# Kernel optimization log

Measured on AMD Instinct MI355X. Metric: run time of the kernel, lower is better.

## Reference

```python
import jax, jax.numpy as jnp
import numpy as np


def setup_inputs() -> dict:
    key = jax.random.key(0)
    x = jax.random.normal(key, (128, 256, 32, 32), dtype=jnp.float32)
    return {"x": x, "iter_num": 5}


def reference(x, iter_num):
    # x: (B, C, H, W)
    B, C, H, W = x.shape
    N = H * W
    xr = x.reshape(B, C, N)
    # Covariance pooling: X @ I_hat @ X^T == (1/N) * Xc @ Xc^T  (I_hat = I/N - J/N^2)
    xc = xr - xr.mean(axis=2, keepdims=True)
    cov = jnp.einsum('bcn,bdn->bcd', xc, xc) / N  # (B, C, C)

    # Newton-Schulz iterative matrix square root
    I = jnp.eye(C, dtype=x.dtype)
    I3 = 3.0 * I
    trace = jnp.trace(cov, axis1=1, axis2=2)[:, None, None]  # norm_A = tr(cov)
    A = cov / trace
    ZY = 0.5 * (I3 - A)
    Y = A @ ZY
    Z = ZY
    for _ in range(1, iter_num - 1):
        ZY = 0.5 * (I3 - Z @ Y)
        Y = Y @ ZY
        Z = ZY @ Z
    YZY = 0.5 * (Y @ (I3 - Z @ Y))
    sqrtm = YZY * jnp.sqrt(trace)  # (B, C, C)

    # Upper-triangular vectorization (row-major, including diagonal)
    r, c = np.triu_indices(C)
    idx = jnp.asarray(r * C + c)
    return sqrtm.reshape(B, C * C)[:, idx]  # (B, C*(C+1)//2)
```

## Files before the change

kernel.cpp:

```cpp
#include <hip/hip_runtime.h>
#include <hip/hip_fp16.h>


typedef _Float16 half8 __attribute__((ext_vector_type(8)));
typedef _Float16 half4 __attribute__((ext_vector_type(4)));
typedef float f32x4 __attribute__((ext_vector_type(4)));

#define OUTPB 32896

__device__ __forceinline__ void gl_lds16(const void* g, void* l) {
  __builtin_amdgcn_global_load_lds(
      (const __attribute__((address_space(1))) void*)g,
      (__attribute__((address_space(3))) void*)l, 16, 0, 0);
}

#define VMB(N) asm volatile("s_waitcnt vmcnt(" #N ")\n\ts_barrier" ::: "memory")
#define LKB()  asm volatile("s_waitcnt lgkmcnt(0)\n\ts_barrier" ::: "memory")

__device__ __forceinline__ void tile_pq(int t, int& p, int& q) {
  p = (t > 3) + (t > 6) + (t > 8);
  int base = p * 4 - (p * (p - 1)) / 2;
  q = p + (t - base);
}

__device__ __forceinline__ half8 cvt8(float4 a, float4 b) {
  half8 h;
  h[0] = (_Float16)a.x; h[1] = (_Float16)a.y; h[2] = (_Float16)a.z; h[3] = (_Float16)a.w;
  h[4] = (_Float16)b.x; h[5] = (_Float16)b.y; h[6] = (_Float16)b.z; h[7] = (_Float16)b.w;
  return h;
}

__device__ __forceinline__ void mfma64(const _Float16* lA, const _Float16* lB,
                                       f32x4 (&acc)[2][2], int wr, int wc,
                                       int lr, int lk) {
#pragma unroll
  for (int ks = 0; ks < 2; ++ks) {
    half8 af[2], bf[2];
#pragma unroll
    for (int m = 0; m < 2; ++m) {
      int row = wr * 32 + m * 16 + lr;
      int kc = (ks * 4 + lk) ^ (row & 7);
      af[m] = *(const half8*)&lA[row * 64 + kc * 8];
    }
#pragma unroll
    for (int n = 0; n < 2; ++n) {
      int row = wc * 32 + n * 16 + lr;
      int kc = (ks * 4 + lk) ^ (row & 7);
      bf[n] = *(const half8*)&lB[row * 64 + kc * 8];
    }
    __builtin_amdgcn_s_setprio(1);
#pragma unroll
    for (int m = 0; m < 2; ++m)
#pragma unroll
      for (int n = 0; n < 2; ++n)
        acc[m][n] = __builtin_amdgcn_mfma_f32_16x16x32_f16(af[m], bf[n], acc[m][n], 0, 0, 0);
    __builtin_amdgcn_s_setprio(0);
  }
}

template <typename F>
__device__ __forceinline__ void store_sym(F f, _Float16* D, size_t boff, int p, int q,
    bool mirror, _Float16* ldsT, f32x4 (&acc)[2][2],
    int wr, int wc, int lr, int lk, int tid) {
#pragma unroll
  for (int m = 0; m < 2; ++m)
#pragma unroll
    for (int n = 0; n < 2; ++n) {
      int il0 = wr * 32 + m * 16 + lk * 4;
      int jl = wc * 32 + n * 16 + lr;
      half4 v4;
#pragma unroll
      for (int r = 0; r < 4; ++r) {
        _Float16 v = f(acc[m][n][r], p * 64 + il0 + r, q * 64 + jl);
        v4[r] = v;
        if (mirror) ldsT[(il0 + r) * 64 + (jl ^ (((il0 + r) & 7) << 3))] = v;
      }
      *(half4*)&D[boff + (size_t)(q * 64 + jl) * 256 + p * 64 + il0] = v4;
    }
  if (mirror) {
    __syncthreads();
#pragma unroll
    for (int pp = 0; pp < 2; ++pp) {
      int u = pp * 256 + tid;
      int im = u >> 3, cu = u & 7;
      half8 v8 = *(const half8*)&ldsT[im * 64 + ((cu ^ (im & 7)) << 3)];
      *(half8*)&D[boff + (size_t)(p * 64 + im) * 256 + q * 64 + cu * 8] = v8;
    }
  }
}

__global__ __launch_bounds__(256, 2) void k_cov(const float* __restrict__ x,
                                                _Float16* __restrict__ covh,
                                                float* __restrict__ trPart) {
  __shared__ _Float16 lds[32768];
  __shared__ float sred[4];

  const int lin = blockIdx.x + 3 * blockIdx.y;
  const int cid = (lin & 7) * 48 + (lin >> 3);
  const int b = cid / 3, t = cid - 3 * b;
  const int p = (t == 1), q = (t != 0);
  const bool diag = (t < 2);
  const int tid = threadIdx.x, w = tid >> 6, lane = tid & 63;
  const int wr = w >> 1, wc = w & 1, lr = lane & 15, lk = lane >> 4;

  const float* Ab = x + ((size_t)b * 256 + p * 128) * 1024;
  const float* Bb = x + ((size_t)b * 256 + q * 128) * 1024;

  float4 la[4][2], lb[4][2];
  f32x4 acc[4][4] = {};
  f32x4 rsA[4] = {}, rsB[4] = {};
  half8 ones;
#pragma unroll
  for (int i = 0; i < 8; ++i) ones[i] = (_Float16)1.0f;

  auto LOAD = [&](int kk) {
#pragma unroll
    for (int i = 0; i < 4; ++i) {
      int u = i * 256 + tid;
      int row = u >> 3, c8 = u & 7;
      int kc = c8 ^ (row & 7);
      const float* sa = Ab + (size_t)row * 1024 + kk * 64 + kc * 8;
      la[i][0] = *(const float4*)sa; la[i][1] = *(const float4*)(sa + 4);
      if (!diag) {
        const float* sb = Bb + (size_t)row * 1024 + kk * 64 + kc * 8;
        lb[i][0] = *(const float4*)sb; lb[i][1] = *(const float4*)(sb + 4);
      }
    }
  };
  auto WRITE = [&](int buf) {
#pragma unroll
    for (int i = 0; i < 4; ++i) {
      int u = i * 256 + tid;
      *(half8*)&lds[buf * 8192 + u * 8] = cvt8(la[i][0], la[i][1]);
      if (!diag) *(half8*)&lds[16384 + buf * 8192 + u * 8] = cvt8(lb[i][0], lb[i][1]);
    }
  };
  auto STEP = [&](const _Float16* lA, const _Float16* lB) {
#pragma unroll
    for (int ks = 0; ks < 2; ++ks) {
      half8 af[4], bf[4];
#pragma unroll
      for (int m = 0; m < 4; ++m) {
        int row = wr * 64 + m * 16 + lr;
        int kc = (ks * 4 + lk) ^ (row & 7);
        af[m] = *(const half8*)&lA[row * 64 + kc * 8];
      }
#pragma unroll
      for (int n = 0; n < 4; ++n) {
        int row = wc * 64 + n * 16 + lr;
        int kc = (ks * 4 + lk) ^ (row & 7);
        bf[n] = *(const half8*)&lB[row * 64 + kc * 8];
      }
      __builtin_amdgcn_s_setprio(1);
#pragma unroll
      for (int m = 0; m < 4; ++m)
        rsA[m] = __builtin_amdgcn_mfma_f32_16x16x32_f16(af[m], ones, rsA[m], 0, 0, 0);
#pragma unroll
      for (int n = 0; n < 4; ++n)
        rsB[n] = __builtin_amdgcn_mfma_f32_16x16x32_f16(ones, bf[n], rsB[n], 0, 0, 0);
#pragma unroll
      for (int m = 0; m < 4; ++m)
#pragma unroll
        for (int n = 0; n < 4; ++n)
          acc[m][n] = __builtin_amdgcn_mfma_f32_16x16x32_f16(af[m], bf[n], acc[m][n], 0, 0, 0);
      __builtin_amdgcn_s_setprio(0);
    }
  };

  LOAD(0); WRITE(0); LOAD(1);
  __syncthreads();
#pragma unroll 1
  for (int kk = 0; kk < 16; ++kk) {
    int cur = kk & 1;
    STEP(&lds[cur * 8192], diag ? &lds[cur * 8192] : &lds[16384 + cur * 8192]);
    if (kk < 15) {
      WRITE(cur ^ 1);
      if (kk < 14) LOAD(kk + 2);
    }
    __syncthreads();
  }

  const float inv = 1.f / 1024.f;
  if (diag) {
    float tp = 0.f;
#pragma unroll
    for (int m = 0; m < 4; ++m)
#pragma unroll
      for (int n = 0; n < 4; ++n)
#pragma unroll
        for (int r = 0; r < 4; ++r) {
          int il = wr * 64 + m * 16 + lk * 4 + r, jl = wc * 64 + n * 16 + lr;
          if (il == jl) tp += (acc[m][n][r] - rsA[m][r] * rsB[n][0] * inv) * inv;
        }
#pragma unroll
    for (int o = 32; o; o >>= 1) tp += __shfl_down(tp, o);
    if (lane == 0) sred[w] = tp;
    __syncthreads();
    if (tid == 0) trPart[b * 2 + p] = sred[0] + sred[1] + sred[2] + sred[3];
  }

  const size_t boff = (size_t)b * 65536;
#pragma unroll
  for (int m = 0; m < 4; ++m)
#pragma unroll
    for (int n = 0; n < 4; ++n) {
      int il0 = wr * 64 + m * 16 + lk * 4;
      int jl = wc * 64 + n * 16 + lr;
      half4 v4;
#pragma unroll
      for (int r = 0; r < 4; ++r) {
        int il = il0 + r;
        float cv = (acc[m][n][r] - rsA[m][r] * rsB[n][0] * inv) * inv;
        v4[r] = (_Float16)cv;
        if (!diag) lds[il * 128 + (((jl >> 3) ^ (il & 7)) << 3) + (jl & 7)] = v4[r];
      }
      *(half4*)&covh[boff + (size_t)(q * 128 + jl) * 256 + p * 128 + il0] = v4;
    }
  if (!diag) {
    __syncthreads();
#pragma unroll
    for (int pp = 0; pp < 8; ++pp) {
      int u = pp * 256 + tid;
      int im = u >> 4, cu = u & 15;
      half8 v8 = *(const half8*)&lds[im * 128 + ((cu ^ (im & 7)) << 3)];
      *(half8*)&covh[boff + (size_t)(p * 128 + im) * 256 + q * 128 + cu * 8] = v8;
    }
  }
}

enum { EPI_S2 = 0, EPI_ZY = 1, EPI_OUT = 2 };

struct GP {
  const _Float16 *A0, *B0;
  _Float16 *D0, *D1;
  const _Float16* covh;
  const float* trP;
  float* outF;
};

template <int EPI>
__global__ __launch_bounds__(256, 4) void k_gemm(GP g) {
  __shared__ _Float16 lds[16384];

  const int lin = blockIdx.x + 10 * blockIdx.y;
  const int cid = (lin & 7) * 160 + (lin >> 3);
  const int b = cid / 10, t = cid - 10 * b;
  int p, q; tile_pq(t, p, q);
  const bool diag = (p == q);
  const bool share = diag && (EPI == EPI_S2);
  const int tid = threadIdx.x, w = tid >> 6, lane = tid & 63;
  const int wr = w >> 1, wc = w & 1, lr = lane & 15, lk = lane >> 4;

  const size_t boff = (size_t)b * 65536;
  const _Float16* Ap = g.A0 + boff + (size_t)p * 64 * 256;
  const _Float16* Bp = ((EPI == EPI_S2) ? g.A0 : g.B0) + boff + (size_t)q * 64 * 256;

  f32x4 acc[2][2] = {};

  auto stageH = [&](const _Float16* panel, int buf, int base, int kk) {
#pragma unroll
    for (int i = 0; i < 2; ++i) {
      int s = (w * 2 + i) * 64 + lane;
      int row = s >> 3, cst = s & 7;
      int kc = cst ^ (row & 7);
      gl_lds16(panel + (size_t)row * 256 + kk * 64 + kc * 8,
               &lds[base + buf * 4096 + (w * 2 + i) * 512]);
    }
  };

  stageH(Ap, 0, 0, 0);
  if (!share) stageH(Bp, 0, 8192, 0);
#pragma unroll 1
  for (int kk = 0; kk < 4; ++kk) {
    int cur = kk & 1;
    if (kk < 3) {
      stageH(Ap, cur ^ 1, 0, kk + 1);
      if (!share) {
        stageH(Bp, cur ^ 1, 8192, kk + 1);
        VMB(4);
      } else {
        VMB(2);
      }
    } else {
      VMB(0);
    }
    mfma64(&lds[cur * 4096], share ? &lds[cur * 4096] : &lds[8192 + cur * 4096],
           acc, wr, wc, lr, lk);
    LKB();
  }

  if constexpr (EPI == EPI_ZY) {
    store_sym([&](float a, int i, int j) {
                return (_Float16)((i == j ? 1.5f : 0.f) - 0.5f * a);
              }, g.D0, boff, p, q, !diag, lds, acc, wr, wc, lr, lk, tid);
  } else if constexpr (EPI == EPI_S2) {
    float tv = g.trP[b * 2] + g.trP[b * 2 + 1];
    float it1 = 1.f / tv;
    _Float16* TY = lds;
    _Float16* TZ = lds + 4096;
#pragma unroll
    for (int m = 0; m < 2; ++m)
#pragma unroll
      for (int n = 0; n < 2; ++n) {
        int il0 = wr * 32 + m * 16 + lk * 4;
        int jl = wc * 32 + n * 16 + lr;
        half4 c4 = *(const half4*)&g.covh[boff + (size_t)(q * 64 + jl) * 256 + p * 64 + il0];
        half4 y4, z4;
#pragma unroll
        for (int r = 0; r < 4; ++r) {
          int i = p * 64 + il0 + r, j = q * 64 + jl;
          float c = (float)c4[r];
          y4[r] = (_Float16)(1.5f * c * it1 - 0.5f * acc[m][n][r] * it1 * it1);
          z4[r] = (_Float16)((i == j ? 1.5f : 0.f) - 0.5f * c * it1);
          if (!diag) {
            int sp = (il0 + r) * 64 + (jl ^ (((il0 + r) & 7) << 3));
            TY[sp] = y4[r]; TZ[sp] = z4[r];
          }
        }
        *(half4*)&g.D0[boff + (size_t)(q * 64 + jl) * 256 + p * 64 + il0] = y4;
        *(half4*)&g.D1[boff + (size_t)(q * 64 + jl) * 256 + p * 64 + il0] = z4;
      }
    if (!diag) {
      __syncthreads();
#pragma unroll
      for (int pp = 0; pp < 2; ++pp) {
        int u = pp * 256 + tid;
        int im = u >> 3, cu = u & 7;
        half8 vy = *(const half8*)&TY[im * 64 + ((cu ^ (im & 7)) << 3)];
        half8 vz = *(const half8*)&TZ[im * 64 + ((cu ^ (im & 7)) << 3)];
        *(half8*)&g.D0[boff + (size_t)(p * 64 + im) * 256 + q * 64 + cu * 8] = vy;
        *(half8*)&g.D1[boff + (size_t)(p * 64 + im) * 256 + q * 64 + cu * 8] = vz;
      }
    }
  } else {
    float tv = g.trP[b * 2] + g.trP[b * 2 + 1];
    float st = sqrtf(tv);
#pragma unroll
    for (int m = 0; m < 2; ++m)
#pragma unroll
      for (int n = 0; n < 2; ++n)
#pragma unroll
        for (int r = 0; r < 4; ++r) {
          int i = p * 64 + wr * 32 + m * 16 + lk * 4 + r;
          int j = q * 64 + wc * 32 + n * 16 + lr;
          if (i <= j) {
            int idx = j + i * 256 - (i * (i + 1)) / 2;
            g.outF[(size_t)b * OUTPB + idx] = acc[m][n][r] * st;
          }
        }
  }
}

struct YZP {
  const _Float16 *Y, *Z, *W;
  _Float16 *Yn, *Zn;
};

__global__ __launch_bounds__(256, 3) void k_yzm(YZP g) {
  __shared__ _Float16 lds[24576];

  const int lin = blockIdx.x + 10 * blockIdx.y;
  const int cid = (lin & 7) * 160 + (lin >> 3);
  const int b = cid / 10, t = cid - 10 * b;
  int p, q; tile_pq(t, p, q);
  const bool diag = (p == q);
  const int tid = threadIdx.x, w = tid >> 6, lane = tid & 63;
  const int wr = w >> 1, wc = w & 1, lr = lane & 15, lk = lane >> 4;

  const size_t boff = (size_t)b * 65536;
  const _Float16* Yp = g.Y + boff + (size_t)p * 64 * 256;
  const _Float16* Zp = g.Z + boff + (size_t)p * 64 * 256;
  const _Float16* Wp = g.W + boff + (size_t)q * 64 * 256;

  f32x4 accY[2][2] = {}, accZ[2][2] = {};

  auto stageH = [&](const _Float16* panel, int buf, int base, int kk) {
#pragma unroll
    for (int i = 0; i < 2; ++i) {
      int s = (w * 2 + i) * 64 + lane;
      int row = s >> 3, cst = s & 7;
      int kc = cst ^ (row & 7);
      gl_lds16(panel + (size_t)row * 256 + kk * 64 + kc * 8,
               &lds[base + buf * 4096 + (w * 2 + i) * 512]);
    }
  };

  auto step = [&](const _Float16* lY, const _Float16* lZ, const _Float16* lW) {
#pragma unroll
    for (int ks = 0; ks < 2; ++ks) {
      half8 yf[2], zf[2], wf[2];
#pragma unroll
      for (int m = 0; m < 2; ++m) {
        int row = wr * 32 + m * 16 + lr;
        int kc = (ks * 4 + lk) ^ (row & 7);
        yf[m] = *(const half8*)&lY[row * 64 + kc * 8];
        zf[m] = *(const half8*)&lZ[row * 64 + kc * 8];
      }
#pragma unroll
      for (int n = 0; n < 2; ++n) {
        int row = wc * 32 + n * 16 + lr;
        int kc = (ks * 4 + lk) ^ (row & 7);
        wf[n] = *(const half8*)&lW[row * 64 + kc * 8];
      }
      __builtin_amdgcn_s_setprio(1);
#pragma unroll
      for (int m = 0; m < 2; ++m)
#pragma unroll
        for (int n = 0; n < 2; ++n) {
          accY[m][n] = __builtin_amdgcn_mfma_f32_16x16x32_f16(yf[m], wf[n], accY[m][n], 0, 0, 0);
          accZ[m][n] = __builtin_amdgcn_mfma_f32_16x16x32_f16(zf[m], wf[n], accZ[m][n], 0, 0, 0);
        }
      __builtin_amdgcn_s_setprio(0);
    }
  };

  stageH(Yp, 0, 0, 0); stageH(Zp, 0, 8192, 0); stageH(Wp, 0, 16384, 0);
#pragma unroll 1
  for (int kk = 0; kk < 4; ++kk) {
    int cur = kk & 1;
    if (kk < 3) {
      stageH(Yp, cur ^ 1, 0, kk + 1);
      stageH(Zp, cur ^ 1, 8192, kk + 1);
      stageH(Wp, cur ^ 1, 16384, kk + 1);
      VMB(6);
    } else {
      VMB(0);
    }
    step(&lds[cur * 4096], &lds[8192 + cur * 4096], &lds[16384 + cur * 4096]);
    LKB();
  }

  _Float16* TY = lds;
  _Float16* TZ = lds + 4096;
#pragma unroll
  for (int m = 0; m < 2; ++m)
#pragma unroll
    for (int n = 0; n < 2; ++n) {
      int il0 = wr * 32 + m * 16 + lk * 4;
      int jl = wc * 32 + n * 16 + lr;
      half4 y4, z4;
#pragma unroll
      for (int r = 0; r < 4; ++r) {
        y4[r] = (_Float16)accY[m][n][r];
        z4[r] = (_Float16)accZ[m][n][r];
        if (!diag) {
          int sp = (il0 + r) * 64 + (jl ^ (((il0 + r) & 7) << 3));
          TY[sp] = y4[r]; TZ[sp] = z4[r];
        }
      }
      *(half4*)&g.Yn[boff + (size_t)(q * 64 + jl) * 256 + p * 64 + il0] = y4;
      *(half4*)&g.Zn[boff + (size_t)(q * 64 + jl) * 256 + p * 64 + il0] = z4;
    }
  if (!diag) {
    __syncthreads();
#pragma unroll
    for (int pp = 0; pp < 2; ++pp) {
      int u = pp * 256 + tid;
      int im = u >> 3, cu = u & 7;
      half8 vy = *(const half8*)&TY[im * 64 + ((cu ^ (im & 7)) << 3)];
      half8 vz = *(const half8*)&TZ[im * 64 + ((cu ^ (im & 7)) << 3)];
      *(half8*)&g.Yn[boff + (size_t)(p * 64 + im) * 256 + q * 64 + cu * 8] = vy;
      *(half8*)&g.Zn[boff + (size_t)(p * 64 + im) * 256 + q * 64 + cu * 8] = vz;
    }
  }
}

extern "C" void kernel_launch(void* const* d_in, const int* in_sizes, int n_in,
                              void* d_out, int out_size, void* d_ws, size_t ws_size,
                              hipStream_t stream) {
  const float* x = (const float*)d_in[0];
  float* outF = (float*)d_out;

  char* ws = (char*)d_ws;
  const size_t MATB = (size_t)128 * 65536 * sizeof(_Float16);
  _Float16* covh = (_Float16*)ws;
  _Float16* Y0   = (_Float16*)(ws + MATB);
  _Float16* Z0   = (_Float16*)(ws + 2 * MATB);
  _Float16* Y1   = (_Float16*)(ws + 3 * MATB);
  _Float16* Z1   = (_Float16*)(ws + 4 * MATB);
  float* trP     = (float*)(ws + 5 * MATB);

  dim3 g3(3, 128), g10(10, 128);

  k_cov<<<g3, 256, 0, stream>>>(x, covh, trP);

  {
    GP a{};
    a.A0 = covh; a.D0 = Y0; a.D1 = Z0;
    a.covh = covh; a.trP = trP;
    k_gemm<EPI_S2><<<g10, 256, 0, stream>>>(a);
  }

  _Float16 *Yc = Y0, *Zc = Z0, *Yn = Y1, *Zn = Z1;
  for (int itn = 0; itn < 3; ++itn) {
    GP a{};
    a.A0 = Zc; a.B0 = Yc; a.D0 = covh;
    k_gemm<EPI_ZY><<<g10, 256, 0, stream>>>(a);
    YZP r{};
    r.Y = Yc; r.Z = Zc; r.W = covh; r.Yn = Yn; r.Zn = Zn;
    k_yzm<<<g10, 256, 0, stream>>>(r);
    _Float16* t0 = Yc; Yc = Yn; Yn = t0;
    _Float16* t1 = Zc; Zc = Zn; Zn = t1;
  }
  {
    GP a{};
    a.A0 = Zc; a.B0 = Yc; a.D0 = covh;
    k_gemm<EPI_ZY><<<g10, 256, 0, stream>>>(a);
    GP o{};
    o.A0 = Yc; o.B0 = covh; o.trP = trP; o.outF = outF;
    k_gemm<EPI_OUT><<<g10, 256, 0, stream>>>(o);
  }
}
```

Measured before the change: 159.0 us.

## Fuse each Newton-Schulz iteration into one column-panel kernel

Replaces the two-kernel-per-iteration scheme (ZY = 1.5I - 0.5 Z@Y written to global, then Y@ZY and ZY@Z) with a single kernel per iteration. Each block owns a 64-column panel of one batch: it computes the ZY panel into LDS, then multiplies Y and Z by it, and writes the new Y and Z columns. This removes the global round trip of ZY and half the launches. The cost is that symmetric-tile reuse is lost, so full 256x64 panels are computed with a 4x128 grid at lower occupancy, and the Y and Z panels are streamed again for each column block.

```diff
diff --git a/kernel.cpp b/kernel.cpp
--- a/kernel.cpp
+++ b/kernel.cpp
@@ -58,205 +58,9 @@
   }
 }
 
-template <typename F>
-__device__ __forceinline__ void store_sym(F f, _Float16* D, size_t boff, int p, int q,
-    bool mirror, _Float16* ldsT, f32x4 (&acc)[2][2],
-    int wr, int wc, int lr, int lk, int tid) {
-#pragma unroll
-  for (int m = 0; m < 2; ++m)
-#pragma unroll
-    for (int n = 0; n < 2; ++n) {
-      int il0 = wr * 32 + m * 16 + lk * 4;
-      int jl = wc * 32 + n * 16 + lr;
-      half4 v4;
-#pragma unroll
-      for (int r = 0; r < 4; ++r) {
-        _Float16 v = f(acc[m][n][r], p * 64 + il0 + r, q * 64 + jl);
-        v4[r] = v;
-        if (mirror) ldsT[(il0 + r) * 64 + (jl ^ (((il0 + r) & 7) << 3))] = v;
-      }
-      *(half4*)&D[boff + (size_t)(q * 64 + jl) * 256 + p * 64 + il0] = v4;
-    }
-  if (mirror) {
-    __syncthreads();
-#pragma unroll
-    for (int pp = 0; pp < 2; ++pp) {
-      int u = pp * 256 + tid;
-      int im = u >> 3, cu = u & 7;
-      half8 v8 = *(const half8*)&ldsT[im * 64 + ((cu ^ (im & 7)) << 3)];
-      *(half8*)&D[boff + (size_t)(p * 64 + im) * 256 + q * 64 + cu * 8] = v8;
-    }
-  }
-}
-
-__global__ __launch_bounds__(256, 2) void k_cov(const float* __restrict__ x,
-                                                _Float16* __restrict__ covh,
-                                                float* __restrict__ trPart) {
-  __shared__ _Float16 lds[32768];
-  __shared__ float sred[4];
-
-  const int lin = blockIdx.x + 3 * blockIdx.y;
-  const int cid = (lin & 7) * 48 + (lin >> 3);
-  const int b = cid / 3, t = cid - 3 * b;
-  const int p = (t == 1), q = (t != 0);
-  const bool diag = (t < 2);
-  const int tid = threadIdx.x, w = tid >> 6, lane = tid & 63;
-  const int wr = w >> 1, wc = w & 1, lr = lane & 15, lk = lane >> 4;
-
-  const float* Ab = x + ((size_t)b * 256 + p * 128) * 1024;
-  const float* Bb = x + ((size_t)b * 256 + q * 128) * 1024;
-
-  float4 la[4][2], lb[4][2];
-  f32x4 acc[4][4] = {};
-  f32x4 rsA[4] = {}, rsB[4] = {};
-  half8 ones;
-#pragma unroll
-  for (int i = 0; i < 8; ++i) ones[i] = (_Float16)1.0f;
-
-  auto LOAD = [&](int kk) {
-#pragma unroll
-    for (int i = 0; i < 4; ++i) {
-      int u = i * 256 + tid;
-      int row = u >> 3, c8 = u & 7;
-      int kc = c8 ^ (row & 7);
-      const float* sa = Ab + (size_t)row * 1024 + kk * 64 + kc * 8;
-      la[i][0] = *(const float4*)sa; la[i][1] = *(const float4*)(sa + 4);
-      if (!diag) {
-        const float* sb = Bb + (size_t)row * 1024 + kk * 64 + kc * 8;
-        lb[i][0] = *(const float4*)sb; lb[i][1] = *(const float4*)(sb + 4);
-      }
-    }
-  };
-  auto WRITE = [&](int buf) {
-#pragma unroll
-    for (int i = 0; i < 4; ++i) {
-      int u = i * 256 + tid;
-      *(half8*)&lds[buf * 8192 + u * 8] = cvt8(la[i][0], la[i][1]);
-      if (!diag) *(half8*)&lds[16384 + buf * 8192 + u * 8] = cvt8(lb[i][0], lb[i][1]);
-    }
-  };
-  auto STEP = [&](const _Float16* lA, const _Float16* lB) {
-#pragma unroll
-    for (int ks = 0; ks < 2; ++ks) {
-      half8 af[4], bf[4];
-#pragma unroll
-      for (int m = 0; m < 4; ++m) {
-        int row = wr * 64 + m * 16 + lr;
-        int kc = (ks * 4 + lk) ^ (row & 7);
-        af[m] = *(const half8*)&lA[row * 64 + kc * 8];
-      }
-#pragma unroll
-      for (int n = 0; n < 4; ++n) {
-        int row = wc * 64 + n * 16 + lr;
-        int kc = (ks * 4 + lk) ^ (row & 7);
-        bf[n] = *(const half8*)&lB[row * 64 + kc * 8];
-      }
-      __builtin_amdgcn_s_setprio(1);
-#pragma unroll
-      for (int m = 0; m < 4; ++m)
-        rsA[m] = __builtin_amdgcn_mfma_f32_16x16x32_f16(af[m], ones, rsA[m], 0, 0, 0);
-#pragma unroll
-      for (int n = 0; n < 4; ++n)
-        rsB[n] = __builtin_amdgcn_mfma_f32_16x16x32_f16(ones, bf[n], rsB[n], 0, 0, 0);
-#pragma unroll
-      for (int m = 0; m < 4; ++m)
-#pragma unroll
-        for (int n = 0; n < 4; ++n)
-          acc[m][n] = __builtin_amdgcn_mfma_f32_16x16x32_f16(af[m], bf[n], acc[m][n], 0, 0, 0);
-      __builtin_amdgcn_s_setprio(0);
-    }
-  };
-
-  LOAD(0); WRITE(0); LOAD(1);
-  __syncthreads();
-#pragma unroll 1
-  for (int kk = 0; kk < 16; ++kk) {
-    int cur = kk & 1;
-    STEP(&lds[cur * 8192], diag ? &lds[cur * 8192] : &lds[16384 + cur * 8192]);
-    if (kk < 15) {
-      WRITE(cur ^ 1);
-      if (kk < 14) LOAD(kk + 2);
-    }
-    __syncthreads();
-  }
-
-  const float inv = 1.f / 1024.f;
-  if (diag) {
-    float tp = 0.f;
-#pragma unroll
-    for (int m = 0; m < 4; ++m)
-#pragma unroll
-      for (int n = 0; n < 4; ++n)
-#pragma unroll
-        for (int r = 0; r < 4; ++r) {
-          int il = wr * 64 + m * 16 + lk * 4 + r, jl = wc * 64 + n * 16 + lr;
-          if (il == jl) tp += (acc[m][n][r] - rsA[m][r] * rsB[n][0] * inv) * inv;
-        }
-#pragma unroll
-    for (int o = 32; o; o >>= 1) tp += __shfl_down(tp, o);
-    if (lane == 0) sred[w] = tp;
-    __syncthreads();
-    if (tid == 0) trPart[b * 2 + p] = sred[0] + sred[1] + sred[2] + sred[3];
-  }
-
-  const size_t boff = (size_t)b * 65536;
-#pragma unroll
-  for (int m = 0; m < 4; ++m)
-#pragma unroll
-    for (int n = 0; n < 4; ++n) {
-      int il0 = wr * 64 + m * 16 + lk * 4;
-      int jl = wc * 64 + n * 16 + lr;
-      half4 v4;
-#pragma unroll
-      for (int r = 0; r < 4; ++r) {
-        int il = il0 + r;
-        float cv = (acc[m][n][r] - rsA[m][r] * rsB[n][0] * inv) * inv;
-        v4[r] = (_Float16)cv;
-        if (!diag) lds[il * 128 + (((jl >> 3) ^ (il & 7)) << 3) + (jl & 7)] = v4[r];
-      }
-      *(half4*)&covh[boff + (size_t)(q * 128 + jl) * 256 + p * 128 + il0] = v4;
-    }
-  if (!diag) {
-    __syncthreads();
-#pragma unroll
-    for (int pp = 0; pp < 8; ++pp) {
-      int u = pp * 256 + tid;
-      int im = u >> 4, cu = u & 15;
-      half8 v8 = *(const half8*)&lds[im * 128 + ((cu ^ (im & 7)) << 3)];
-      *(half8*)&covh[boff + (size_t)(p * 128 + im) * 256 + q * 128 + cu * 8] = v8;
-    }
-  }
-}
-
-enum { EPI_S2 = 0, EPI_ZY = 1, EPI_OUT = 2 };
-
-struct GP {
-  const _Float16 *A0, *B0;
-  _Float16 *D0, *D1;
-  const _Float16* covh;
-  const float* trP;
-  float* outF;
-};
-
-template <int EPI>
-__global__ __launch_bounds__(256, 4) void k_gemm(GP g) {
-  __shared__ _Float16 lds[16384];
-
-  const int lin = blockIdx.x + 10 * blockIdx.y;
-  const int cid = (lin & 7) * 160 + (lin >> 3);
-  const int b = cid / 10, t = cid - 10 * b;
-  int p, q; tile_pq(t, p, q);
-  const bool diag = (p == q);
-  const bool share = diag && (EPI == EPI_S2);
-  const int tid = threadIdx.x, w = tid >> 6, lane = tid & 63;
-  const int wr = w >> 1, wc = w & 1, lr = lane & 15, lk = lane >> 4;
-
-  const size_t boff = (size_t)b * 65536;
-  const _Float16* Ap = g.A0 + boff + (size_t)p * 64 * 256;
-  const _Float16* Bp = ((EPI == EPI_S2) ? g.A0 : g.B0) + boff + (size_t)q * 64 * 256;
-
-  f32x4 acc[2][2] = {};
-
+__device__ __forceinline__ void gemm64(const _Float16* Ap, const _Float16* Bp,
+    bool share, _Float16* lds, f32x4 (&acc)[2][2], int tid) {
+  const int w = tid >> 6, lane = tid & 63;
   auto stageH = [&](const _Float16* panel, int buf, int base, int kk) {
 #pragma unroll
     for (int i = 0; i < 2; ++i) {
@@ -267,7 +71,7 @@
                &lds[base + buf * 4096 + (w * 2 + i) * 512]);
     }
   };
-
+  const int wr = w >> 1, wc = w & 1, lr = lane & 15, lk = lane >> 4;
   stageH(Ap, 0, 0, 0);
   if (!share) stageH(Bp, 0, 8192, 0);
 #pragma unroll 1
@@ -288,77 +92,152 @@
            acc, wr, wc, lr, lk);
     LKB();
   }
-
-  if constexpr (EPI == EPI_ZY) {
-    store_sym([&](float a, int i, int j) {
-                return (_Float16)((i == j ? 1.5f : 0.f) - 0.5f * a);
-              }, g.D0, boff, p, q, !diag, lds, acc, wr, wc, lr, lk, tid);
-  } else if constexpr (EPI == EPI_S2) {
-    float tv = g.trP[b * 2] + g.trP[b * 2 + 1];
-    float it1 = 1.f / tv;
-    _Float16* TY = lds;
-    _Float16* TZ = lds + 4096;
-#pragma unroll
-    for (int m = 0; m < 2; ++m)
-#pragma unroll
-      for (int n = 0; n < 2; ++n) {
-        int il0 = wr * 32 + m * 16 + lk * 4;
-        int jl = wc * 32 + n * 16 + lr;
-        half4 c4 = *(const half4*)&g.covh[boff + (size_t)(q * 64 + jl) * 256 + p * 64 + il0];
-        half4 y4, z4;
+}
+
+__global__ __launch_bounds__(256, 2) void k_cov(const float* __restrict__ x,
+                                                _Float16* __restrict__ covh,
+                                                float* __restrict__ trPart) {
+  __shared__ _Float16 lds[32768];
+  __shared__ float sred[4];
+
+  const int lin = blockIdx.x + 3 * blockIdx.y;
+  const int cid = (lin & 7) * 48 + (lin >> 3);
+  const int b = cid / 3, t = cid - 3 * b;
+  const int p = (t == 1), q = (t != 0);
+  const bool diag = (t < 2);
+  const int tid = threadIdx.x, w = tid >> 6, lane = tid & 63;
+  const int wr = w >> 1, wc = w & 1, lr = lane & 15, lk = lane >> 4;
+
+  const float* Ab = x + ((size_t)b * 256 + p * 128) * 1024;
+  const float* Bb = x + ((size_t)b * 256 + q * 128) * 1024;
+
+  float4 la[4][2], lb[4][2];
+  f32x4 acc[4][4] = {};
+  f32x4 rsA[4] = {}, rsB[4] = {};
+  half8 ones;
+#pragma unroll
+  for (int i = 0; i < 8; ++i) ones[i] = (_Float16)1.0f;
+
+  auto LOAD = [&](int kk) {
+#pragma unroll
+    for (int i = 0; i < 4; ++i) {
+      int u = i * 256 + tid;
+      int row = u >> 3, c8 = u & 7;
+      int kc = c8 ^ (row & 7);
+      const float* sa = Ab + (size_t)row * 1024 + kk * 64 + kc * 8;
+      la[i][0] = *(const float4*)sa; la[i][1] = *(const float4*)(sa + 4);
+      if (!diag) {
+        const float* sb = Bb + (size_t)row * 1024 + kk * 64 + kc * 8;
+        lb[i][0] = *(const float4*)sb; lb[i][1] = *(const float4*)(sb + 4);
+      }
+    }
+  };
+  auto WRITE = [&](int buf) {
+#pragma unroll
+    for (int i = 0; i < 4; ++i) {
+      int u = i * 256 + tid;
+      *(half8*)&lds[buf * 8192 + u * 8] = cvt8(la[i][0], la[i][1]);
+      if (!diag) *(half8*)&lds[16384 + buf * 8192 + u * 8] = cvt8(lb[i][0], lb[i][1]);
+    }
+  };
+  auto STEP = [&](const _Float16* lA, const _Float16* lB) {
+#pragma unroll
+    for (int ks = 0; ks < 2; ++ks) {
+      half8 af[4], bf[4];
+#pragma unroll
+      for (int m = 0; m < 4; ++m) {
+        int row = wr * 64 + m * 16 + lr;
+        int kc = (ks * 4 + lk) ^ (row & 7);
+        af[m] = *(const half8*)&lA[row * 64 + kc * 8];
+      }
+#pragma unroll
+      for (int n = 0; n < 4; ++n) {
+        int row = wc * 64 + n * 16 + lr;
+        int kc = (ks * 4 + lk) ^ (row & 7);
+        bf[n] = *(const half8*)&lB[row * 64 + kc * 8];
+      }
+      __builtin_amdgcn_s_setprio(1);
+#pragma unroll
+      for (int m = 0; m < 4; ++m)
+        rsA[m] = __builtin_amdgcn_mfma_f32_16x16x32_f16(af[m], ones, rsA[m], 0, 0, 0);
+#pragma unroll
+      for (int n = 0; n < 4; ++n)
+        rsB[n] = __builtin_amdgcn_mfma_f32_16x16x32_f16(ones, bf[n], rsB[n], 0, 0, 0);
+#pragma unroll
+      for (int m = 0; m < 4; ++m)
+#pragma unroll
+        for (int n = 0; n < 4; ++n)
+          acc[m][n] = __builtin_amdgcn_mfma_f32_16x16x32_f16(af[m], bf[n], acc[m][n], 0, 0, 0);
+      __builtin_amdgcn_s_setprio(0);
+    }
+  };
+
+  LOAD(0); WRITE(0); LOAD(1);
+  __syncthreads();
+#pragma unroll 1
+  for (int kk = 0; kk < 16; ++kk) {
+    int cur = kk & 1;
+    STEP(&lds[cur * 8192], diag ? &lds[cur * 8192] : &lds[16384 + cur * 8192]);
+    if (kk < 15) {
+      WRITE(cur ^ 1);
+      if (kk < 14) LOAD(kk + 2);
+    }
+    __syncthreads();
+  }
+
+  const float inv = 1.f / 1024.f;
+  if (diag) {
+    float tp = 0.f;
+#pragma unroll
+    for (int m = 0; m < 4; ++m)
+#pragma unroll
+      for (int n = 0; n < 4; ++n)
 #pragma unroll
         for (int r = 0; r < 4; ++r) {
-          int i = p * 64 + il0 + r, j = q * 64 + jl;
-          float c = (float)c4[r];
-          y4[r] = (_Float16)(1.5f * c * it1 - 0.5f * acc[m][n][r] * it1 * it1);
-          z4[r] = (_Float16)((i == j ? 1.5f : 0.f) - 0.5f * c * it1);
-          if (!diag) {
-            int sp = (il0 + r) * 64 + (jl ^ (((il0 + r) & 7) << 3));
-            TY[sp] = y4[r]; TZ[sp] = z4[r];
-          }
+          int il = wr * 64 + m * 16 + lk * 4 + r, jl = wc * 64 + n * 16 + lr;
+          if (il == jl) tp += (acc[m][n][r] - rsA[m][r] * rsB[n][0] * inv) * inv;
         }
-        *(half4*)&g.D0[boff + (size_t)(q * 64 + jl) * 256 + p * 64 + il0] = y4;
-        *(half4*)&g.D1[boff + (size_t)(q * 64 + jl) * 256 + p * 64 + il0] = z4;
-      }
-    if (!diag) {
-      __syncthreads();
-#pragma unroll
-      for (int pp = 0; pp < 2; ++pp) {
-        int u = pp * 256 + tid;
-        int im = u >> 3, cu = u & 7;
-        half8 vy = *(const half8*)&TY[im * 64 + ((cu ^ (im & 7)) << 3)];
-        half8 vz = *(const half8*)&TZ[im * 64 + ((cu ^ (im & 7)) << 3)];
-        *(half8*)&g.D0[boff + (size_t)(p * 64 + im) * 256 + q * 64 + cu * 8] = vy;
-        *(half8*)&g.D1[boff + (size_t)(p * 64 + im) * 256 + q * 64 + cu * 8] = vz;
-      }
-    }
-  } else {
-    float tv = g.trP[b * 2] + g.trP[b * 2 + 1];
-    float st = sqrtf(tv);
-#pragma unroll
-    for (int m = 0; m < 2; ++m)
-#pragma unroll
-      for (int n = 0; n < 2; ++n)
-#pragma unroll
-        for (int r = 0; r < 4; ++r) {
-          int i = p * 64 + wr * 32 + m * 16 + lk * 4 + r;
-          int j = q * 64 + wc * 32 + n * 16 + lr;
-          if (i <= j) {
-            int idx = j + i * 256 - (i * (i + 1)) / 2;
-            g.outF[(size_t)b * OUTPB + idx] = acc[m][n][r] * st;
-          }
-        }
-  }
-}
-
-struct YZP {
-  const _Float16 *Y, *Z, *W;
-  _Float16 *Yn, *Zn;
-};
-
-__global__ __launch_bounds__(256, 3) void k_yzm(YZP g) {
-  __shared__ _Float16 lds[24576];
-
+#pragma unroll
+    for (int o = 32; o; o >>= 1) tp += __shfl_down(tp, o);
+    if (lane == 0) sred[w] = tp;
+    __syncthreads();
+    if (tid == 0) trPart[b * 2 + p] = sred[0] + sred[1] + sred[2] + sred[3];
+  }
+
+  const size_t boff = (size_t)b * 65536;
+#pragma unroll
+  for (int m = 0; m < 4; ++m)
+#pragma unroll
+    for (int n = 0; n < 4; ++n) {
+      int il0 = wr * 64 + m * 16 + lk * 4;
+      int jl = wc * 64 + n * 16 + lr;
+      half4 v4;
+#pragma unroll
+      for (int r = 0; r < 4; ++r) {
+        int il = il0 + r;
+        float cv = (acc[m][n][r] - rsA[m][r] * rsB[n][0] * inv) * inv;
+        v4[r] = (_Float16)cv;
+        if (!diag) lds[il * 128 + (((jl >> 3) ^ (il & 7)) << 3) + (jl & 7)] = v4[r];
+      }
+      *(half4*)&covh[boff + (size_t)(q * 128 + jl) * 256 + p * 128 + il0] = v4;
+    }
+  if (!diag) {
+    __syncthreads();
+#pragma unroll
+    for (int pp = 0; pp < 8; ++pp) {
+      int u = pp * 256 + tid;
+      int im = u >> 4, cu = u & 15;
+      half8 v8 = *(const half8*)&lds[im * 128 + ((cu ^ (im & 7)) << 3)];
+      *(half8*)&covh[boff + (size_t)(p * 128 + im) * 256 + q * 128 + cu * 8] = v8;
+    }
+  }
+}
+
+__global__ __launch_bounds__(256, 4) void k_s2(const _Float16* __restrict__ covh,
+                                               const float* __restrict__ trP,
+                                               _Float16* __restrict__ Y0,
+                                               _Float16* __restrict__ Z0) {
+  __shared__ _Float16 lds[16384];
   const int lin = blockIdx.x + 10 * blockIdx.y;
   const int cid = (lin & 7) * 160 + (lin >> 3);
   const int b = cid / 10, t = cid - 10 * b;
@@ -366,70 +245,14 @@
   const bool diag = (p == q);
   const int tid = threadIdx.x, w = tid >> 6, lane = tid & 63;
   const int wr = w >> 1, wc = w & 1, lr = lane & 15, lk = lane >> 4;
-
   const size_t boff = (size_t)b * 65536;
-  const _Float16* Yp = g.Y + boff + (size_t)p * 64 * 256;
-  const _Float16* Zp = g.Z + boff + (size_t)p * 64 * 256;
-  const _Float16* Wp = g.W + boff + (size_t)q * 64 * 256;
-
-  f32x4 accY[2][2] = {}, accZ[2][2] = {};
-
-  auto stageH = [&](const _Float16* panel, int buf, int base, int kk) {
-#pragma unroll
-    for (int i = 0; i < 2; ++i) {
-      int s = (w * 2 + i) * 64 + lane;
-      int row = s >> 3, cst = s & 7;
-      int kc = cst ^ (row & 7);
-      gl_lds16(panel + (size_t)row * 256 + kk * 64 + kc * 8,
-               &lds[base + buf * 4096 + (w * 2 + i) * 512]);
-    }
-  };
-
-  auto step = [&](const _Float16* lY, const _Float16* lZ, const _Float16* lW) {
-#pragma unroll
-    for (int ks = 0; ks < 2; ++ks) {
-      half8 yf[2], zf[2], wf[2];
-#pragma unroll
-      for (int m = 0; m < 2; ++m) {
-        int row = wr * 32 + m * 16 + lr;
-        int kc = (ks * 4 + lk) ^ (row & 7);
-        yf[m] = *(const half8*)&lY[row * 64 + kc * 8];
-        zf[m] = *(const half8*)&lZ[row * 64 + kc * 8];
-      }
-#pragma unroll
-      for (int n = 0; n < 2; ++n) {
-        int row = wc * 32 + n * 16 + lr;
-        int kc = (ks * 4 + lk) ^ (row & 7);
-        wf[n] = *(const half8*)&lW[row * 64 + kc * 8];
-      }
-      __builtin_amdgcn_s_setprio(1);
-#pragma unroll
-      for (int m = 0; m < 2; ++m)
-#pragma unroll
-        for (int n = 0; n < 2; ++n) {
-          accY[m][n] = __builtin_amdgcn_mfma_f32_16x16x32_f16(yf[m], wf[n], accY[m][n], 0, 0, 0);
-          accZ[m][n] = __builtin_amdgcn_mfma_f32_16x16x32_f16(zf[m], wf[n], accZ[m][n], 0, 0, 0);
-        }
-      __builtin_amdgcn_s_setprio(0);
-    }
-  };
-
-  stageH(Yp, 0, 0, 0); stageH(Zp, 0, 8192, 0); stageH(Wp, 0, 16384, 0);
-#pragma unroll 1
-  for (int kk = 0; kk < 4; ++kk) {
-    int cur = kk & 1;
-    if (kk < 3) {
-      stageH(Yp, cur ^ 1, 0, kk + 1);
-      stageH(Zp, cur ^ 1, 8192, kk + 1);
-      stageH(Wp, cur ^ 1, 16384, kk + 1);
-      VMB(6);
-    } else {
-      VMB(0);
-    }
-    step(&lds[cur * 4096], &lds[8192 + cur * 4096], &lds[16384 + cur * 4096]);
-    LKB();
-  }
-
+
+  f32x4 acc[2][2] = {};
+  gemm64(covh + boff + (size_t)p * 64 * 256, covh + boff + (size_t)q * 64 * 256,
+         diag, lds, acc, tid);
+
+  float tv = trP[b * 2] + trP[b * 2 + 1];
+  float it1 = 1.f / tv;
   _Float16* TY = lds;
   _Float16* TZ = lds + 4096;
 #pragma unroll
@@ -438,18 +261,21 @@
     for (int n = 0; n < 2; ++n) {
       int il0 = wr * 32 + m * 16 + lk * 4;
       int jl = wc * 32 + n * 16 + lr;
+      half4 c4 = *(const half4*)&covh[boff + (size_t)(q * 64 + jl) * 256 + p * 64 + il0];
       half4 y4, z4;
 #pragma unroll
       for (int r = 0; r < 4; ++r) {
-        y4[r] = (_Float16)accY[m][n][r];
-        z4[r] = (_Float16)accZ[m][n][r];
+        int i = p * 64 + il0 + r, j = q * 64 + jl;
+        float c = (float)c4[r];
+        y4[r] = (_Float16)(1.5f * c * it1 - 0.5f * acc[m][n][r] * it1 * it1);
+        z4[r] = (_Float16)((i == j ? 1.5f : 0.f) - 0.5f * c * it1);
         if (!diag) {
           int sp = (il0 + r) * 64 + (jl ^ (((il0 + r) & 7) << 3));
           TY[sp] = y4[r]; TZ[sp] = z4[r];
         }
       }
-      *(half4*)&g.Yn[boff + (size_t)(q * 64 + jl) * 256 + p * 64 + il0] = y4;
-      *(half4*)&g.Zn[boff + (size_t)(q * 64 + jl) * 256 + p * 64 + il0] = z4;
+      *(half4*)&Y0[boff + (size_t)(q * 64 + jl) * 256 + p * 64 + il0] = y4;
+      *(half4*)&Z0[boff + (size_t)(q * 64 + jl) * 256 + p * 64 + il0] = z4;
     }
   if (!diag) {
     __syncthreads();
@@ -459,9 +285,196 @@
       int im = u >> 3, cu = u & 7;
       half8 vy = *(const half8*)&TY[im * 64 + ((cu ^ (im & 7)) << 3)];
       half8 vz = *(const half8*)&TZ[im * 64 + ((cu ^ (im & 7)) << 3)];
-      *(half8*)&g.Yn[boff + (size_t)(p * 64 + im) * 256 + q * 64 + cu * 8] = vy;
-      *(half8*)&g.Zn[boff + (size_t)(p * 64 + im) * 256 + q * 64 + cu * 8] = vz;
-    }
+      *(half8*)&Y0[boff + (size_t)(p * 64 + im) * 256 + q * 64 + cu * 8] = vy;
+      *(half8*)&Z0[boff + (size_t)(p * 64 + im) * 256 + q * 64 + cu * 8] = vz;
+    }
+  }
+}
+
+
+#define IT_STAGE_RES(SRC)                                                  \
+  {                                                                        \
+    _Pragma("unroll") for (int i = 0; i < 8; ++i) {                        \
+      int s = i * 256 + tid;                                               \
+      int row = s >> 5, cp = s & 31;                                       \
+      int c = cp ^ (row & 7);                                              \
+      gl_lds16((SRC) + (size_t)(q * 64 + row) * 256 + c * 8, &lds[s * 8]); \
+    }                                                                      \
+  }
+
+struct ITP {
+  const _Float16 *Y, *Z;
+  _Float16 *Yn, *Zn;
+  const float* trP;
+  float* outF;
+};
+
+template <bool FINAL>
+__global__ __launch_bounds__(256, 2) void k_it(ITP P) {
+  __shared__ _Float16 lds[32768];
+  const int lin = blockIdx.x + 4 * blockIdx.y;
+  const int cid = (lin & 7) * 64 + (lin >> 3);
+  const int b = cid >> 2, q = cid & 3;
+  const int tid = threadIdx.x, w = tid >> 6, lane = tid & 63;
+  const int lr = lane & 15, lk = lane >> 4;
+  const size_t boff = (size_t)b * 65536;
+  const _Float16* Yg = P.Y + boff;
+  const _Float16* Zg = P.Z + boff;
+
+  auto stage = [&](const _Float16* M, int buf, int kk) {
+#pragma unroll
+    for (int i = 0; i < 4; ++i) {
+      int s = i * 256 + tid;
+      int row = s >> 2, cp = s & 3;
+      int c = cp ^ (row & 3);
+      gl_lds16(M + (size_t)row * 256 + kk * 32 + c * 8,
+               &lds[16384 + buf * 8192 + s * 8]);
+    }
+  };
+
+  f32x4 acc[4][4];
+  auto zero = [&]() {
+#pragma unroll
+    for (int m = 0; m < 4; ++m)
+#pragma unroll
+      for (int n = 0; n < 4; ++n) {
+        f32x4 z = {0.f, 0.f, 0.f, 0.f};
+        acc[m][n] = z;
+      }
+  };
+
+  auto stepRA = [&](int kk, int cur) {
+    half8 af[4], bf[4];
+    const _Float16* sb = &lds[16384 + cur * 8192];
+#pragma unroll
+    for (int m = 0; m < 4; ++m) {
+      int row = m * 16 + lr;
+      int c = (kk * 4 + lk) ^ (row & 7);
+      af[m] = *(const half8*)&lds[row * 256 + c * 8];
+    }
+#pragma unroll
+    for (int n = 0; n < 4; ++n) {
+      int row = w * 64 + n * 16 + lr;
+      int cp = lk ^ (row & 3);
+      bf[n] = *(const half8*)&sb[row * 32 + cp * 8];
+    }
+    __builtin_amdgcn_s_setprio(1);
+#pragma unroll
+    for (int m = 0; m < 4; ++m)
+#pragma unroll
+      for (int n = 0; n < 4; ++n)
+        acc[m][n] = __builtin_amdgcn_mfma_f32_16x16x32_f16(af[m], bf[n], acc[m][n], 0, 0, 0);
+    __builtin_amdgcn_s_setprio(0);
+  };
+  auto stepRB = [&](int kk, int cur) {
+    half8 af[4], bf[4];
+    const _Float16* sa = &lds[16384 + cur * 8192];
+#pragma unroll
+    for (int m = 0; m < 4; ++m) {
+      int row = w * 64 + m * 16 + lr;
+      int cp = lk ^ (row & 3);
+      af[m] = *(const half8*)&sa[row * 32 + cp * 8];
+    }
+#pragma unroll
+    for (int n = 0; n < 4; ++n) {
+      int row = n * 16 + lr;
+      int c = (kk * 4 + lk) ^ (row & 7);
+      bf[n] = *(const half8*)&lds[row * 256 + c * 8];
+    }
+    __builtin_amdgcn_s_setprio(1);
+#pragma unroll
+    for (int m = 0; m < 4; ++m)
+#pragma unroll
+      for (int n = 0; n < 4; ++n)
+        acc[m][n] = __builtin_amdgcn_mfma_f32_16x16x32_f16(af[m], bf[n], acc[m][n], 0, 0, 0);
+    __builtin_amdgcn_s_setprio(0);
+  };
+
+  zero();
+  IT_STAGE_RES(Zg);
+  stage(Yg, 0, 0);
+#pragma unroll 1
+  for (int kk = 0; kk < 8; ++kk) {
+    int cur = kk & 1;
+    if (kk < 7) { stage(Yg, cur ^ 1, kk + 1); VMB(4); } else { VMB(0); }
+    stepRA(kk, cur);
+    LKB();
+  }
+#pragma unroll
+  for (int m = 0; m < 4; ++m)
+#pragma unroll
+    for (int n = 0; n < 4; ++n) {
+      int kcol = w * 64 + n * 16 + lr;
+#pragma unroll
+      for (int r = 0; r < 4; ++r) {
+        int j = m * 16 + lk * 4 + r;
+        float v = (kcol == q * 64 + j ? 1.5f : 0.f) - 0.5f * acc[m][n][r];
+        lds[j * 256 + (((kcol >> 3) ^ (j & 7)) << 3) + (kcol & 7)] = (_Float16)v;
+      }
+    }
+  __syncthreads();
+
+  zero();
+  stage(Yg, 0, 0);
+#pragma unroll 1
+  for (int kk = 0; kk < 8; ++kk) {
+    int cur = kk & 1;
+    if (kk < 7) { stage(Yg, cur ^ 1, kk + 1); VMB(4); } else { VMB(0); }
+    stepRB(kk, cur);
+    LKB();
+  }
+
+  if constexpr (!FINAL) {
+#pragma unroll
+    for (int m = 0; m < 4; ++m)
+#pragma unroll
+      for (int n = 0; n < 4; ++n) {
+        int jg = q * 64 + n * 16 + lr;
+        int i0 = w * 64 + m * 16 + lk * 4;
+        half4 v4;
+#pragma unroll
+        for (int r = 0; r < 4; ++r) v4[r] = (_Float16)acc[m][n][r];
+        *(half4*)&P.Yn[boff + (size_t)jg * 256 + i0] = v4;
+      }
+
+    zero();
+    stage(Zg, 0, 0);
+#pragma unroll 1
+    for (int kk = 0; kk < 8; ++kk) {
+      int cur = kk & 1;
+      if (kk < 7) { stage(Zg, cur ^ 1, kk + 1); VMB(4); } else { VMB(0); }
+      stepRB(kk, cur);
+      LKB();
+    }
+#pragma unroll
+    for (int m = 0; m < 4; ++m)
+#pragma unroll
+      for (int n = 0; n < 4; ++n) {
+        int jg = q * 64 + n * 16 + lr;
+        int i0 = w * 64 + m * 16 + lk * 4;
+        half4 v4;
+#pragma unroll
+        for (int r = 0; r < 4; ++r) v4[r] = (_Float16)acc[m][n][r];
+        *(half4*)&P.Zn[boff + (size_t)jg * 256 + i0] = v4;
+      }
+  } else {
+    float tv = P.trP[b * 2] + P.trP[b * 2 + 1];
+    float st = sqrtf(tv);
+#pragma unroll
+    for (int m = 0; m < 4; ++m)
+#pragma unroll
+      for (int n = 0; n < 4; ++n) {
+        int jg = q * 64 + n * 16 + lr;
+        int i0 = w * 64 + m * 16 + lk * 4;
+#pragma unroll
+        for (int r = 0; r < 4; ++r) {
+          int i = i0 + r;
+          if (i <= jg) {
+            int idx = jg + i * 256 - (i * (i + 1)) / 2;
+            P.outF[(size_t)b * OUTPB + idx] = acc[m][n][r] * st;
+          }
+        }
+      }
   }
 }
 
@@ -480,34 +493,22 @@
   _Float16* Z1   = (_Float16*)(ws + 4 * MATB);
   float* trP     = (float*)(ws + 5 * MATB);
 
-  dim3 g3(3, 128), g10(10, 128);
+  dim3 g3(3, 128), g10(10, 128), g4(4, 128);
 
   k_cov<<<g3, 256, 0, stream>>>(x, covh, trP);
-
-  {
-    GP a{};
-    a.A0 = covh; a.D0 = Y0; a.D1 = Z0;
-    a.covh = covh; a.trP = trP;
-    k_gemm<EPI_S2><<<g10, 256, 0, stream>>>(a);
-  }
+  k_s2<<<g10, 256, 0, stream>>>(covh, trP, Y0, Z0);
 
   _Float16 *Yc = Y0, *Zc = Z0, *Yn = Y1, *Zn = Z1;
   for (int itn = 0; itn < 3; ++itn) {
-    GP a{};
-    a.A0 = Zc; a.B0 = Yc; a.D0 = covh;
-    k_gemm<EPI_ZY><<<g10, 256, 0, stream>>>(a);
-    YZP r{};
-    r.Y = Yc; r.Z = Zc; r.W = covh; r.Yn = Yn; r.Zn = Zn;
-    k_yzm<<<g10, 256, 0, stream>>>(r);
+    ITP p{};
+    p.Y = Yc; p.Z = Zc; p.Yn = Yn; p.Zn = Zn;
+    k_it<false><<<g4, 256, 0, stream>>>(p);
     _Float16* t0 = Yc; Yc = Yn; Yn = t0;
     _Float16* t1 = Zc; Zc = Zn; Zn = t1;
   }
   {
-    GP a{};
-    a.A0 = Zc; a.B0 = Yc; a.D0 = covh;
-    k_gemm<EPI_ZY><<<g10, 256, 0, stream>>>(a);
-    GP o{};
-    o.A0 = Yc; o.B0 = covh; o.trP = trP; o.outF = outF;
-    k_gemm<EPI_OUT><<<g10, 256, 0, stream>>>(o);
-  }
-}
+    ITP p{};
+    p.Y = Yc; p.Z = Zc; p.trP = trP; p.outF = outF;
+    k_it<true><<<g4, 256, 0, stream>>>(p);
+  }
+}
```

Result: no change. 158.5 us (-0.3%).
